# Optimization experiments

Hardware: AMD Instinct MI355X
Metric: run time of the kernel (lower is better)

The kernel has to match this reference:

```python
import jax, jax.numpy as jnp
import numpy as np

POS_THRESH = 0.5
NEG_THRESH = 0.3
MIN_ANCHOR = 3
N_ANCHOR = 500000
N_GT = 200


def _iou_matrix(a, g):
    # a: [N,4], g: [M,4], boxes as (x1,y1,x2,y2)
    area_a = (a[:, 2] - a[:, 0]) * (a[:, 3] - a[:, 1])          # [N]
    area_g = (g[:, 2] - g[:, 0]) * (g[:, 3] - g[:, 1])          # [M]
    lt = jnp.maximum(a[:, None, :2], g[None, :, :2])            # [N,M,2]
    rb = jnp.minimum(a[:, None, 2:], g[None, :, 2:])            # [N,M,2]
    wh = jnp.clip(rb - lt, 0.0)
    inter = wh[..., 0] * wh[..., 1]                              # [N,M]
    return inter / (area_a[:, None] + area_g[None, :] - inter)


def _make_boxes(key, n, coord_max, size_min, size_max):
    kc, ks = jax.random.split(key)
    c = jax.random.uniform(kc, (n, 2), jnp.float32, 0.0, coord_max)
    s = jax.random.uniform(ks, (n, 2), jnp.float32, size_min, size_max)
    return jnp.concatenate([c - 0.5 * s, c + 0.5 * s], axis=1)


def setup_inputs() -> dict:
    key = jax.random.key(0)
    ka, kg = jax.random.split(key)
    anchor = _make_boxes(ka, N_ANCHOR, 1024.0, 8.0, 128.0)
    gt = _make_boxes(kg, N_GT, 1024.0, 16.0, 256.0)
    return {"anchor": anchor, "gt": gt}


def reference(anchor, gt):
    n, m = anchor.shape[0], gt.shape[0]
    iou_mat = _iou_matrix(anchor, gt)                            # [N,M]
    max_iou = jnp.max(iou_mat, axis=1)                           # [N]
    max_idx = jnp.argmax(iou_mat, axis=1).astype(jnp.int32)      # [N] (first max, like torch)
    assign = jnp.full((n,), -2, dtype=jnp.int32)
    assign = jnp.where(max_iou < NEG_THRESH, -1, assign)
    assign = jnp.where(max_iou > POS_THRESH, max_idx, assign)

    # per-GT top-k anchors (iou_mat.T : [M,N])
    vals, ranks = jax.lax.top_k(iou_mat.T, MIN_ANCHOR)           # [M,K]
    low = jnp.sum(vals > POS_THRESH, axis=1) < MIN_ANCHOR        # [M] gt lacking enough positives
    # claim[m,k]: gt m claims anchor ranks[m,k]. k==0 always (best anchor forced);
    # others only if gt is low-quality and iou > 0.1
    claim = (jnp.arange(MIN_ANCHOR)[None, :] == 0) | (low[:, None] & (vals > 0.1))
    gt_idx = jnp.broadcast_to(jnp.arange(m, dtype=jnp.int32)[:, None], (m, MIN_ANCHOR))
    claim_val = jnp.where(claim, gt_idx, -1)                     # [M,K]
    # original python loop runs gt idx in increasing order, later overwrites earlier
    # -> final winner for a contested anchor is the MAX claiming gt index: scatter-max
    forced = jnp.full((n,), -1, dtype=jnp.int32).at[ranks.reshape(-1)].max(claim_val.reshape(-1))
    assign = jnp.where(forced >= 0, forced, assign)
    return assign
```

## Files before the change

kernel.cpp:

```cpp
#include <hip/hip_runtime.h>
#include <stdint.h>


typedef unsigned int u32;
typedef unsigned short u16;
typedef unsigned long long u64;

#define POS_THRESH 0.5f
#define NEG_THRESH 0.3f
#define CLAIM_THRESH 0.1f

constexpr int NCX = 32, NCY = 32, NCELL = NCX * NCY;
constexpr float INV_CELL = 0.03125f;
constexpr float MARGIN = 64.5f;
constexpr int MPAD = 256;
constexpr int NSTRIPE = 10;
constexpr int CPAD = 16;
constexpr int HSLOTS = 1024;
constexpr int HB = 128;

#define INS3(t0, t1, t2, k) do {                                  \
    if ((k) > (t2)) {                                             \
        if ((k) > (t0))      { t2 = t1; t1 = t0; t0 = (k); }      \
        else if ((k) > (t1)) { t2 = t1; t1 = (k); }               \
        else                 { t2 = (k); }                        \
    } } while (0)

#define IOU_EVAL(a, areaA, g, areaG, inter, iou) {                \
    float ltx = fmaxf(a.x, g.x), lty = fmaxf(a.y, g.y);           \
    float rbx = fminf(a.z, g.z), rby = fminf(a.w, g.w);           \
    float ww = fmaxf(rbx - ltx, 0.0f);                            \
    float hh = fmaxf(rby - lty, 0.0f);                            \
    inter = ww * hh;                                              \
    iou = 0.0f;                                                   \
    if (inter > 0.0f) iou = inter / ((areaA + areaG) - inter);    \
}

__device__ __forceinline__ u64 shfl_xor_u64(u64 x, int mask) {
    int lo = __shfl_xor((int)(u32)x, mask, 64);
    int hi = __shfl_xor((int)(u32)(x >> 32), mask, 64);
    return ((u64)(u32)hi << 32) | (u32)lo;
}

__device__ __forceinline__ int cell_of(const float4 a) {
    float cx = 0.5f * (a.x + a.z);
    float cy = 0.5f * (a.y + a.w);
    int ix = (int)(cx * INV_CELL);
    int iy = (int)(cy * INV_CELL);
    ix = ix < 0 ? 0 : (ix > NCX - 1 ? NCX - 1 : ix);
    iy = iy < 0 ? 0 : (iy > NCY - 1 ? NCY - 1 : iy);
    return iy * NCX + ix;
}

__device__ __forceinline__ void gt_range(const float4 g, int& clx, int& chx,
                                         int& cly, int& chy) {
    clx = (int)floorf((g.x - MARGIN) * INV_CELL);
    chx = (int)floorf((g.z + MARGIN) * INV_CELL);
    cly = (int)floorf((g.y - MARGIN) * INV_CELL);
    chy = (int)floorf((g.w + MARGIN) * INV_CELL);
    clx = clx < 0 ? 0 : (clx > NCX - 1 ? NCX - 1 : clx);
    chx = chx < 0 ? 0 : (chx > NCX - 1 ? NCX - 1 : chx);
    cly = cly < 0 ? 0 : (cly > NCY - 1 ? NCY - 1 : cly);
    chy = chy < 0 ? 0 : (chy > NCY - 1 ? NCY - 1 : chy);
}

__global__ void __launch_bounds__(256) k_hist(
    const float4* __restrict__ anchor, u32* __restrict__ histPart, int N)
{
    __shared__ u32 h[NCELL];
    const int tid = threadIdx.x;
    for (int c = tid; c < NCELL; c += 256) h[c] = 0;
    __syncthreads();
    for (int i = blockIdx.x * 256 + tid; i < N; i += 256 * HB)
        atomicAdd(&h[cell_of(anchor[i])], 1u);
    __syncthreads();
    u32* mine = histPart + (size_t)blockIdx.x * NCELL;
    for (int c = tid; c < NCELL; c += 256) mine[c] = h[c];
}

__global__ void __launch_bounds__(256) k_scan(
    const u32* __restrict__ histPart, u32* __restrict__ ccPad,
    u32* __restrict__ cellStart, const float4* __restrict__ gt,
    u32* __restrict__ gtCnt, u16* __restrict__ gtIds, int M)
{
    __shared__ u32 s_sum[256];
    __shared__ u32 l_cnt[NCELL];
    const int tid = threadIdx.x;

    u32 c0 = 0, c1 = 0, c2 = 0, c3 = 0;
    for (int b = 0; b < HB; ++b) {
        const u32* p = histPart + (size_t)b * NCELL + tid * 4;
        c0 += p[0]; c1 += p[1]; c2 += p[2]; c3 += p[3];
    }
    s_sum[tid] = c0 + c1 + c2 + c3;
    for (int c = tid; c < NCELL; c += 256) l_cnt[c] = 0;
    __syncthreads();

    for (int off = 1; off < 256; off <<= 1) {
        u32 v = (tid >= off) ? s_sum[tid - off] : 0;
        __syncthreads();
        s_sum[tid] += v;
        __syncthreads();
    }

    u32 base = tid ? s_sum[tid - 1] : 0;
    cellStart[tid * 4 + 0] = base;  ccPad[(tid * 4 + 0) * CPAD] = base;
    base += c0;
    cellStart[tid * 4 + 1] = base;  ccPad[(tid * 4 + 1) * CPAD] = base;
    base += c1;
    cellStart[tid * 4 + 2] = base;  ccPad[(tid * 4 + 2) * CPAD] = base;
    base += c2;
    cellStart[tid * 4 + 3] = base;  ccPad[(tid * 4 + 3) * CPAD] = base;
    if (tid == 255) cellStart[NCELL] = s_sum[255];

    if (tid < M) {
        float4 g = gt[tid];
        int clx, chx, cly, chy;
        gt_range(g, clx, chx, cly, chy);
        for (int iy = cly; iy <= chy; ++iy)
            for (int ix = clx; ix <= chx; ++ix) {
                int c = iy * NCX + ix;
                u32 slot = atomicAdd(&l_cnt[c], 1u);
                gtIds[(size_t)c * M + slot] = (u16)tid;
            }
    }
    __syncthreads();
    for (int c = tid; c < NCELL; c += 256) gtCnt[c] = l_cnt[c];
}

__global__ void __launch_bounds__(256) k_scatter(
    const float4* __restrict__ anchor, u32* __restrict__ ccPad,
    float4* __restrict__ binnedBox, int* __restrict__ binnedIdx, int N)
{
    int i = blockIdx.x * 256 + threadIdx.x;
    if (i >= N) return;
    float4 a = anchor[i];
    u32 pos = atomicAdd(&ccPad[cell_of(a) * CPAD], 1u);
    binnedBox[pos] = a;
    binnedIdx[pos] = i;
}

__global__ void __launch_bounds__(256) k_assign(
    const float4* __restrict__ binnedBox, const int* __restrict__ binnedIdx,
    const float4* __restrict__ gt, const u32* __restrict__ gtCnt,
    const u16* __restrict__ gtIds, int* __restrict__ out, int N, int M)
{
    __shared__ float4 s_g[MPAD];
    __shared__ float  s_ga[MPAD];
    const int tid = threadIdx.x;
    if (tid < M) {
        float4 g = gt[tid];
        s_g[tid]  = g;
        s_ga[tid] = (g.z - g.x) * (g.w - g.y);
    }
    __syncthreads();

    int p = blockIdx.x * 256 + tid;
    if (p >= N) return;
    float4 a  = binnedBox[p];
    int   idx = binnedIdx[p];
    float area_a = (a.z - a.x) * (a.w - a.y);
    int c   = cell_of(a);
    int cnt = (int)gtCnt[c];
    const u16* list = gtIds + (size_t)c * M;

    u64 best = 0;
    for (int k = 0; k < cnt; ++k) {
        int m = list[k];
        float4 g = s_g[m];
        float inter, iou;
        IOU_EVAL(a, area_a, g, s_ga[m], inter, iou);
        if (inter > 0.0f) {
            u64 key = ((u64)__float_as_uint(iou) << 32) | (~(u32)m);
            best = key > best ? key : best;
        }
    }
    u32 ib = (u32)(best >> 32);
    int v = -2;
    if (ib < __float_as_uint(NEG_THRESH)) v = -1;
    if (ib > __float_as_uint(POS_THRESH)) v = (int)(~(u32)best);
    out[idx] = v;
}

__global__ void __launch_bounds__(256) k_top3(
    const float4* __restrict__ binnedBox, const int* __restrict__ binnedIdx,
    const float4* __restrict__ gt, const u32* __restrict__ cellStart,
    u64* __restrict__ partial3, int M)
{
    const int s    = blockIdx.x;
    const int m    = blockIdx.y;
    const int tid  = threadIdx.x;
    const int lane = tid & 63;
    const int w    = tid >> 6;

    float4 g = gt[m];
    float area_g = (g.z - g.x) * (g.w - g.y);
    int clx, chx, cly, chy;
    gt_range(g, clx, chx, cly, chy);

    u64 t0 = 0x00000000FFFFFFFFULL;
    u64 t1 = 0x00000000FFFFFFFEULL;
    u64 t2 = 0x00000000FFFFFFFDULL;

    int q = 0;
    for (int iy = cly; iy <= chy; ++iy)
        for (int ix = clx; ix <= chx; ++ix, ++q) {
            if (q % NSTRIPE != s) continue;
            int c = iy * NCX + ix;
            int cs = (int)cellStart[c];
            int ce = (int)cellStart[c + 1];
            for (int p = cs + tid; p < ce; p += 256) {
                float4 a = binnedBox[p];
                int  idx = binnedIdx[p];
                float area_a = (a.z - a.x) * (a.w - a.y);
                float inter, iou;
                IOU_EVAL(a, area_a, g, area_g, inter, iou);
                if (inter > 0.0f) {
                    u64 key = ((u64)__float_as_uint(iou) << 32) | (~(u32)idx);
                    INS3(t0, t1, t2, key);
                }
            }
        }

    for (int off = 1; off < 64; off <<= 1) {
        u64 o0 = shfl_xor_u64(t0, off);
        u64 o1 = shfl_xor_u64(t1, off);
        u64 o2 = shfl_xor_u64(t2, off);
        INS3(t0, t1, t2, o0);
        INS3(t0, t1, t2, o1);
        INS3(t0, t1, t2, o2);
    }

    __shared__ u64 s_red[4][3];
    if (lane == 0) { s_red[w][0] = t0; s_red[w][1] = t1; s_red[w][2] = t2; }
    __syncthreads();
    if (tid == 0) {
        u64 q0 = 0, q1 = 0, q2 = 0;
        for (int wv = 0; wv < 4; ++wv) {
            INS3(q0, q1, q2, s_red[wv][0]);
            INS3(q0, q1, q2, s_red[wv][1]);
            INS3(q0, q1, q2, s_red[wv][2]);
        }
        size_t b = ((size_t)m * NSTRIPE + s) * 3;
        partial3[b + 0] = q0;
        partial3[b + 1] = q1;
        partial3[b + 2] = q2;
    }
}

__global__ void __launch_bounds__(256) k_claims(
    const u64* __restrict__ partial3, int* __restrict__ out, int M)
{
    __shared__ u64 s_key[3 * MPAD];
    __shared__ u64 h_val[HSLOTS];
    __shared__ u32 h_tag[HSLOTS];
    const int tid = threadIdx.x;

    for (int i = tid; i < HSLOTS; i += 256) { h_val[i] = 0; h_tag[i] = 0; }

    if (tid < M) {
        u64 q0 = 0, q1 = 0, q2 = 0;
        const u64* p = partial3 + (size_t)tid * NSTRIPE * 3;
        for (int c = 0; c < NSTRIPE * 3; ++c) INS3(q0, q1, q2, p[c]);

        float v0 = __uint_as_float((u32)(q0 >> 32));
        float v1 = __uint_as_float((u32)(q1 >> 32));
        float v2 = __uint_as_float((u32)(q2 >> 32));
        u32 a0 = ~(u32)q0;
        u32 a1 = ~(u32)q1;
        u32 a2 = ~(u32)q2;

        int npos = (v0 > POS_THRESH) + (v1 > POS_THRESH) + (v2 > POS_THRESH);
        bool low = npos < 3;

        s_key[tid * 3 + 0] = ((u64)a0 << 32) | (u32)(tid + 1);
        s_key[tid * 3 + 1] = (low && v1 > CLAIM_THRESH)
            ? (((u64)a1 << 32) | (u32)(tid + 1)) : 0ULL;
        s_key[tid * 3 + 2] = (low && v2 > CLAIM_THRESH)
            ? (((u64)a2 << 32) | (u32)(tid + 1)) : 0ULL;
    }
    __syncthreads();

    const int tote = 3 * M;
    for (int e = tid; e < tote; e += 256) {
        u64 my = s_key[e];
        if (my == 0) continue;
        u32 myA = (u32)(my >> 32);
        u32 slot = (myA * 2654435761u) & (HSLOTS - 1);
        while (true) {
            u32 prev = atomicCAS(&h_tag[slot], 0u, myA + 1u);
            if (prev == 0u || prev == myA + 1u) {
                atomicMax(&h_val[slot], my);
                break;
            }
            slot = (slot + 1) & (HSLOTS - 1);
        }
    }
    __syncthreads();
    for (int e = tid; e < tote; e += 256) {
        u64 my = s_key[e];
        if (my == 0) continue;
        u32 myA = (u32)(my >> 32);
        u32 slot = (myA * 2654435761u) & (HSLOTS - 1);
        while (h_tag[slot] != myA + 1u) slot = (slot + 1) & (HSLOTS - 1);
        if (h_val[slot] == my) out[myA] = (int)(my & 0xffffffffULL) - 1;
    }
}

extern "C" void kernel_launch(void* const* d_in, const int* in_sizes, int n_in,
                              void* d_out, int out_size, void* d_ws, size_t ws_size,
                              hipStream_t stream) {
    const float4* anchor = (const float4*)d_in[0];
    const float4* gt     = (const float4*)d_in[1];
    int N = in_sizes[0] / 4;
    int M = in_sizes[1] / 4;
    int* out = (int*)d_out;

    char* ws = (char*)d_ws;
    size_t off = 0;
    auto alloc = [&](size_t bytes, size_t align) -> void* {
        off = (off + align - 1) / align * align;
        void* p = ws + off;
        off += bytes;
        return p;
    };
    u32* histPart   = (u32*)alloc((size_t)HB * NCELL * 4, 64);
    u32* ccPad      = (u32*)alloc((size_t)NCELL * CPAD * 4, 64);
    u32* cellStart  = (u32*)alloc((NCELL + 1) * 4, 4);
    u32* gtCnt      = (u32*)alloc(NCELL * 4, 4);
    u64* partial3   = (u64*)alloc((size_t)M * NSTRIPE * 3 * 8, 8);
    u16* gtIds      = (u16*)alloc((size_t)NCELL * M * 2, 2);
    float4* binnedBox = (float4*)alloc((size_t)N * 16, 16);
    int* binnedIdx    = (int*)alloc((size_t)N * 4, 4);

    int nb = (N + 255) / 256;
    k_hist<<<HB, 256, 0, stream>>>(anchor, histPart, N);
    k_scan<<<1, 256, 0, stream>>>(histPart, ccPad, cellStart, gt, gtCnt,
                                  gtIds, M);
    k_scatter<<<nb, 256, 0, stream>>>(anchor, ccPad, binnedBox, binnedIdx, N);
    k_assign<<<nb, 256, 0, stream>>>(binnedBox, binnedIdx, gt, gtCnt, gtIds,
                                     out, N, M);
    k_top3<<<dim3(NSTRIPE, M), 256, 0, stream>>>(binnedBox, binnedIdx, gt,
                                                 cellStart, partial3, M);
    k_claims<<<1, 256, 0, stream>>>(partial3, out, M);
}
```

Baseline: 117.1 us.

## Fuse scatter with assign and fold claims into last top3 block

Merges the binning scatter into the per-anchor assignment kernel, so each anchor is read once in original order and written to its bin while its best-GT label is computed. The separate claims kernel becomes a last-block-done tail of the top3 kernel, using a global counter reset in k_hist plus a threadfence. This removes two launches and one re-read of the binned arrays. In exchange, assign now runs on unbinned anchors, which gives worse locality over the per-cell GT lists and more wave divergence, and the big claims shared-memory arrays now live in every top3 block, which may lower occupancy.

```diff
diff --git a/kernel.cpp b/kernel.cpp
--- a/kernel.cpp
+++ b/kernel.cpp
@@ -65,10 +65,12 @@
 }
 
 __global__ void __launch_bounds__(256) k_hist(
-    const float4* __restrict__ anchor, u32* __restrict__ histPart, int N)
+    const float4* __restrict__ anchor, u32* __restrict__ histPart,
+    u32* __restrict__ done3, int N)
 {
     __shared__ u32 h[NCELL];
     const int tid = threadIdx.x;
+    if (blockIdx.x == 0 && tid == 0) *done3 = 0;
     for (int c = tid; c < NCELL; c += 256) h[c] = 0;
     __syncthreads();
     for (int i = blockIdx.x * 256 + tid; i < N; i += 256 * HB)
@@ -128,22 +130,12 @@
     for (int c = tid; c < NCELL; c += 256) gtCnt[c] = l_cnt[c];
 }
 
-__global__ void __launch_bounds__(256) k_scatter(
+__global__ void __launch_bounds__(256) k_scatass(
     const float4* __restrict__ anchor, u32* __restrict__ ccPad,
-    float4* __restrict__ binnedBox, int* __restrict__ binnedIdx, int N)
-{
-    int i = blockIdx.x * 256 + threadIdx.x;
-    if (i >= N) return;
-    float4 a = anchor[i];
-    u32 pos = atomicAdd(&ccPad[cell_of(a) * CPAD], 1u);
-    binnedBox[pos] = a;
-    binnedIdx[pos] = i;
-}
-
-__global__ void __launch_bounds__(256) k_assign(
-    const float4* __restrict__ binnedBox, const int* __restrict__ binnedIdx,
     const float4* __restrict__ gt, const u32* __restrict__ gtCnt,
-    const u16* __restrict__ gtIds, int* __restrict__ out, int N, int M)
+    const u16* __restrict__ gtIds,
+    float4* __restrict__ binnedBox, int* __restrict__ binnedIdx,
+    int* __restrict__ out, int N, int M)
 {
     __shared__ float4 s_g[MPAD];
     __shared__ float  s_ga[MPAD];
@@ -155,12 +147,16 @@
     }
     __syncthreads();
 
-    int p = blockIdx.x * 256 + tid;
-    if (p >= N) return;
-    float4 a  = binnedBox[p];
-    int   idx = binnedIdx[p];
+    int i = blockIdx.x * 256 + tid;
+    if (i >= N) return;
+    float4 a = anchor[i];
+    int c = cell_of(a);
+
+    u32 pos = atomicAdd(&ccPad[c * CPAD], 1u);
+    binnedBox[pos] = a;
+    binnedIdx[pos] = i;
+
     float area_a = (a.z - a.x) * (a.w - a.y);
-    int c   = cell_of(a);
     int cnt = (int)gtCnt[c];
     const u16* list = gtIds + (size_t)c * M;
 
@@ -179,13 +175,14 @@
     int v = -2;
     if (ib < __float_as_uint(NEG_THRESH)) v = -1;
     if (ib > __float_as_uint(POS_THRESH)) v = (int)(~(u32)best);
-    out[idx] = v;
-}
-
-__global__ void __launch_bounds__(256) k_top3(
+    out[i] = v;
+}
+
+__global__ void __launch_bounds__(256) k_top3c(
     const float4* __restrict__ binnedBox, const int* __restrict__ binnedIdx,
     const float4* __restrict__ gt, const u32* __restrict__ cellStart,
-    u64* __restrict__ partial3, int M)
+    u64* __restrict__ partial3, u32* __restrict__ done3,
+    int* __restrict__ out, int M)
 {
     const int s    = blockIdx.x;
     const int m    = blockIdx.y;
@@ -232,6 +229,7 @@
     }
 
     __shared__ u64 s_red[4][3];
+    __shared__ int isLast;
     if (lane == 0) { s_red[w][0] = t0; s_red[w][1] = t1; s_red[w][2] = t2; }
     __syncthreads();
     if (tid == 0) {
@@ -245,17 +243,16 @@
         partial3[b + 0] = q0;
         partial3[b + 1] = q1;
         partial3[b + 2] = q2;
-    }
-}
-
-__global__ void __launch_bounds__(256) k_claims(
-    const u64* __restrict__ partial3, int* __restrict__ out, int M)
-{
+        __threadfence();
+        u32 old = atomicAdd(done3, 1u);
+        isLast = (old == (u32)(NSTRIPE * M - 1));
+    }
+    __syncthreads();
+    if (!isLast) return;
+
     __shared__ u64 s_key[3 * MPAD];
     __shared__ u64 h_val[HSLOTS];
     __shared__ u32 h_tag[HSLOTS];
-    const int tid = threadIdx.x;
-
     for (int i = tid; i < HSLOTS; i += 256) { h_val[i] = 0; h_tag[i] = 0; }
 
     if (tid < M) {
@@ -328,19 +325,19 @@
     u32* ccPad      = (u32*)alloc((size_t)NCELL * CPAD * 4, 64);
     u32* cellStart  = (u32*)alloc((NCELL + 1) * 4, 4);
     u32* gtCnt      = (u32*)alloc(NCELL * 4, 4);
+    u32* done3      = (u32*)alloc(64, 64);
     u64* partial3   = (u64*)alloc((size_t)M * NSTRIPE * 3 * 8, 8);
     u16* gtIds      = (u16*)alloc((size_t)NCELL * M * 2, 2);
     float4* binnedBox = (float4*)alloc((size_t)N * 16, 16);
     int* binnedIdx    = (int*)alloc((size_t)N * 4, 4);
 
     int nb = (N + 255) / 256;
-    k_hist<<<HB, 256, 0, stream>>>(anchor, histPart, N);
+    k_hist<<<HB, 256, 0, stream>>>(anchor, histPart, done3, N);
     k_scan<<<1, 256, 0, stream>>>(histPart, ccPad, cellStart, gt, gtCnt,
                                   gtIds, M);
-    k_scatter<<<nb, 256, 0, stream>>>(anchor, ccPad, binnedBox, binnedIdx, N);
-    k_assign<<<nb, 256, 0, stream>>>(binnedBox, binnedIdx, gt, gtCnt, gtIds,
-                                     out, N, M);
-    k_top3<<<dim3(NSTRIPE, M), 256, 0, stream>>>(binnedBox, binnedIdx, gt,
-                                                 cellStart, partial3, M);
-    k_claims<<<1, 256, 0, stream>>>(partial3, out, M);
-}
+    k_scatass<<<nb, 256, 0, stream>>>(anchor, ccPad, gt, gtCnt, gtIds,
+                                      binnedBox, binnedIdx, out, N, M);
+    k_top3c<<<dim3(NSTRIPE, M), 256, 0, stream>>>(binnedBox, binnedIdx, gt,
+                                                  cellStart, partial3, done3,
+                                                  out, M);
+}
```

Result: slower. 164.7 us (+40.7%).
